# Performance work log

Hardware: AMD Instinct MI355X
Metric: run time of the kernel (lower is better)

The kernel has to match this reference:

```python
import jax, jax.numpy as jnp
import numpy as np
import math

H = 16
D_MODEL = 1024
D_K = D_MODEL // H


def setup_inputs() -> dict:
    key = jax.random.key(0)
    ks = jax.random.split(key, 11)
    B, S, D = 4, 2048, D_MODEL
    scale = 1.0 / math.sqrt(D)
    inp = {
        "query": jax.random.normal(ks[0], (B, S, D), jnp.float32),
        "key": jax.random.normal(ks[1], (B, S, D), jnp.float32),
        "value": jax.random.normal(ks[2], (B, S, D), jnp.float32),
        # four Linear(d_model, d_model) layers: Wq, Wk, Wv, Wo (weights stored [in, out])
        "Wq": jax.random.normal(ks[3], (D, D), jnp.float32) * scale,
        "bq": jnp.zeros((D,), jnp.float32),
        "Wk": jax.random.normal(ks[4], (D, D), jnp.float32) * scale,
        "bk": jnp.zeros((D,), jnp.float32),
        "Wv": jax.random.normal(ks[5], (D, D), jnp.float32) * scale,
        "bv": jnp.zeros((D,), jnp.float32),
        "Wo": jax.random.normal(ks[6], (D, D), jnp.float32) * scale,
        "bo": jnp.zeros((D,), jnp.float32),
    }
    return inp


def reference(query, key, value, Wq, bq, Wk, bk, Wv, bv, Wo, bo):
    B, S, D = query.shape
    # QKV projections, split into heads: [B, H, S, d_k]
    def proj(x, W, b):
        return (x @ W + b).reshape(B, -1, H, D_K).transpose(0, 2, 1, 3)

    q = proj(query, Wq, bq)
    k = proj(key, Wk, bk)
    v = proj(value, Wv, bv)

    # scaled dot-product attention (mask=None, dropout p=0 -> identity)
    scores = jnp.einsum("bhqd,bhkd->bhqk", q, k) / math.sqrt(D_K)
    p_attn = jax.nn.softmax(scores, axis=-1)
    x = jnp.einsum("bhqk,bhkd->bhqd", p_attn, v)

    # merge heads and output projection
    x = x.transpose(0, 2, 1, 3).reshape(B, -1, H * D_K)
    return x @ Wo + bo
```

## Files before the change

kernel.cpp:

```cpp
#include <hip/hip_runtime.h>


typedef unsigned short u16;
typedef unsigned int u32;
typedef __attribute__((ext_vector_type(8))) short bfx8;
typedef __attribute__((ext_vector_type(4))) float f32x4;
typedef __attribute__((ext_vector_type(16))) float f32x16;
typedef __attribute__((ext_vector_type(4))) float fx4;
typedef __attribute__((ext_vector_type(8))) u16 u16x8;
typedef __attribute__((ext_vector_type(4))) u16 u16x4;
typedef __attribute__((ext_vector_type(4))) u32 u32x4;

__device__ __forceinline__ u16 f2bf(float f) {
  union { float f; u32 u; } v; v.f = f;
  u32 u = v.u;
  u += 0x7fffu + ((u >> 16) & 1u);
  return (u16)(u >> 16);
}

__device__ __forceinline__ u32 cvtpk(float a, float b) {
  u32 r;
  asm("v_cvt_pk_bf16_f32 %0, %1, %2" : "=v"(r) : "v"(a), "v"(b));
  return r;
}

__device__ __forceinline__ void gl_lds16(const void* g, void* l) {
  __builtin_amdgcn_global_load_lds((const __attribute__((address_space(1))) void*)g,
                                   (__attribute__((address_space(3))) void*)l, 16, 0, 0);
}

__global__ void prep(const float* __restrict__ q, const float* __restrict__ k,
                     const float* __restrict__ v, u16* __restrict__ inBase,
                     const float* __restrict__ W0, const float* __restrict__ W1,
                     const float* __restrict__ W2, const float* __restrict__ W3,
                     u16* __restrict__ WtBase) {
  __shared__ float tile[64][65];
  const int bid = blockIdx.x;
  const int t = threadIdx.x;
  if (bid < 12288) {
    const int z = bid >> 12, xb = bid & 4095;
    const float* in = z == 0 ? q : (z == 1 ? k : v);
    u16* out = inBase + (size_t)z * (8192ull * 1024);
    const int i = (xb * 256 + t) * 8;
    fx4 a = *(const fx4*)(in + i);
    fx4 b = *(const fx4*)(in + i + 4);
    u16x8 o;
    o[0] = f2bf(a[0]); o[1] = f2bf(a[1]); o[2] = f2bf(a[2]); o[3] = f2bf(a[3]);
    o[4] = f2bf(b[0]); o[5] = f2bf(b[1]); o[6] = f2bf(b[2]); o[7] = f2bf(b[3]);
    *(u16x8*)(out + i) = o;
  } else {
    const int wb = bid - 12288;
    const int z = wb >> 8, rem = wb & 255;
    const float* W = z == 0 ? W0 : (z == 1 ? W1 : (z == 2 ? W2 : W3));
    u16* Wt = WtBase + (size_t)z * (1024ull * 1024);
    const int n0 = (rem & 15) << 6, k0 = (rem >> 4) << 6;
    {
      int r = t >> 2, c = (t & 3) << 4;
      const float* src = W + (size_t)(k0 + r) * 1024 + n0 + c;
#pragma unroll
      for (int u = 0; u < 4; ++u) {
        fx4 vv = *(const fx4*)(src + u * 4);
        tile[r][c + u * 4 + 0] = vv[0];
        tile[r][c + u * 4 + 1] = vv[1];
        tile[r][c + u * 4 + 2] = vv[2];
        tile[r][c + u * 4 + 3] = vv[3];
      }
    }
    __syncthreads();
    {
      int nn = t >> 2, j = t & 3;
      u16x8 o0, o1;
#pragma unroll
      for (int e = 0; e < 8; ++e) o0[e] = f2bf(tile[(j << 4) + e][nn]);
#pragma unroll
      for (int e = 0; e < 8; ++e) o1[e] = f2bf(tile[(j << 4) + 8 + e][nn]);
      u16* dst = Wt + (size_t)(n0 + nn) * 1024 + k0 + (j << 4);
      *(u16x8*)dst = o0;
      *(u16x8*)(dst + 8) = o1;
    }
  }
}

template <int EPI>
__device__ __forceinline__ void gemm_body(const u16* __restrict__ A, const u16* __restrict__ Bt,
                                          const float* __restrict__ bias, void* __restrict__ out,
                                          float scale, char* smem, int m0, int n0) {
  const int t = threadIdx.x;
  const int w = t >> 6, l = t & 63;
  const int lg = l >> 4, lr = l & 15;
  const int wr = w >> 1, wc = w & 1;

  f32x4 acc[4][4] = {};

  const int trow = t >> 3;
  const int scb = ((t & 7) << 4) ^ ((trow & 7) << 4);
  const char* gA = (const char*)A + (size_t)(m0 + trow) * 2048;
  const char* gB = (const char*)Bt + (size_t)(n0 + trow) * 2048;

#define GSTAGE(kt, buf)                                                        \
  do {                                                                         \
    _Pragma("unroll")                                                          \
    for (int i = 0; i < 4; ++i) {                                              \
      gl_lds16(gA + (size_t)i * 32 * 2048 + ((kt) << 7) + scb,                 \
               (buf) + (((i << 8) + (w << 6)) << 4));                          \
      gl_lds16(gB + (size_t)i * 32 * 2048 + ((kt) << 7) + scb,                 \
               (buf) + 16384 + (((i << 8) + (w << 6)) << 4));                  \
    }                                                                          \
  } while (0)

  GSTAGE(0, smem);
  __syncthreads();

  for (int kt = 0; kt < 16; ++kt) {
    char* sA = smem + ((kt & 1) << 15);
    char* sB = sA + 16384;
    if (kt < 15) GSTAGE(kt + 1, smem + (((kt + 1) & 1) << 15));

#pragma unroll
    for (int kk = 0; kk < 2; ++kk) {
      const int off = ((kk << 6) + (lg << 4)) ^ ((lr & 7) << 4);
      bfx8 av[4], bv[4];
#pragma unroll
      for (int fi = 0; fi < 4; ++fi)
        av[fi] = *(const bfx8*)(sA + ((wr << 6) + (fi << 4) + lr) * 128 + off);
#pragma unroll
      for (int fj = 0; fj < 4; ++fj)
        bv[fj] = *(const bfx8*)(sB + ((wc << 6) + (fj << 4) + lr) * 128 + off);
#pragma unroll
      for (int fi = 0; fi < 4; ++fi)
#pragma unroll
        for (int fj = 0; fj < 4; ++fj)
          acc[fi][fj] = __builtin_amdgcn_mfma_f32_16x16x32_bf16(av[fi], bv[fj], acc[fi][fj], 0, 0, 0);
    }
    __syncthreads();
  }
#undef GSTAGE

#pragma unroll
  for (int fj = 0; fj < 4; ++fj) {
    const int n = n0 + (wc << 6) + (fj << 4) + lr;
    const float bvl = bias[n];
#pragma unroll
    for (int fi = 0; fi < 4; ++fi) {
      if constexpr (EPI == 2) {
        const int h = n >> 6, d = n & 63;
        const int mm = m0 + (wr << 6) + (fi << 4) + (lg << 2);
        const int b = mm >> 11, s = mm & 2047;
        u16x4 pk4;
#pragma unroll
        for (int r = 0; r < 4; ++r) pk4[r] = f2bf(acc[fi][fj][r] + bvl);
        *(u16x4*)((u16*)out + (size_t)(b * 16 + h) * 131072 + (size_t)d * 2048 + s) = pk4;
      } else {
#pragma unroll
        for (int r = 0; r < 4; ++r) {
          const int m = m0 + (wr << 6) + (fi << 4) + (lg << 2) + r;
          const float val = (acc[fi][fj][r] + bvl) * scale;
          if constexpr (EPI == 0) {
            const int b = m >> 11, s = m & 2047, h = n >> 6, d = n & 63;
            ((u16*)out)[(((size_t)(b * 16 + h) * 2048 + s) << 6) + d] = f2bf(val);
          } else {
            ((float*)out)[((size_t)m << 10) + n] = val;
          }
        }
      }
    }
  }
}

__device__ __forceinline__ void xcd_remap(int& m0, int& n0) {
  const int lin = blockIdx.x + (blockIdx.y << 3);
  const int c = lin & 7, j = lin >> 3;
  m0 = (((j & 7) << 3) + c) << 7;
  n0 = (j >> 3) << 7;
}

__global__ void __launch_bounds__(256, 2)
gemm_qkv(const u16* __restrict__ A0, const u16* __restrict__ Wt0,
         const float* __restrict__ bq, const float* __restrict__ bk,
         const float* __restrict__ bv, u16* __restrict__ out0, u16* __restrict__ vt) {
  __shared__ __align__(16) char smem[65536];
  const int z = blockIdx.z;
  int m0, n0;
  xcd_remap(m0, n0);
  const u16* A = A0 + (size_t)z * (8192ull * 1024);
  const u16* Bt = Wt0 + (size_t)z * (1024ull * 1024);
  if (z == 2) {
    gemm_body<2>(A, Bt, bv, vt, 1.0f, smem, m0, n0);
  } else {
    const float* bias = z == 0 ? bq : bk;
    const float scale = z == 0 ? 0.18033688011112042f : 1.0f;
    gemm_body<0>(A, Bt, bias, out0 + (size_t)z * (8192ull * 1024), scale, smem, m0, n0);
  }
}

__global__ void __launch_bounds__(256, 2)
gemm_o(const u16* __restrict__ A, const u16* __restrict__ Bt,
       const float* __restrict__ bias, float* __restrict__ out) {
  __shared__ __align__(16) char smem[65536];
  int m0, n0;
  xcd_remap(m0, n0);
  gemm_body<1>(A, Bt, bias, out, 1.0f, smem, m0, n0);
}

__global__ void __launch_bounds__(512, 4)
attn_fwd(const u16* __restrict__ Qg, const u16* __restrict__ Kg,
         const u16* __restrict__ Vtg, u16* __restrict__ Og) {
  __shared__ __align__(16) char smem[65536];
  const int t = threadIdx.x;
  const int w = t >> 6, l = t & 63;
  const int l31 = l & 31, hi = l >> 5;

  const int id = blockIdx.x;
  const int xcd = id & 7, slot = id >> 3;
  const int pair = ((slot >> 3) << 3) + xcd;
  const int q0 = (slot & 7) << 8;

  const char* Qb = (const char*)Qg + ((size_t)pair << 18);
  const char* Kb = (const char*)Kg + ((size_t)pair << 18);
  const char* Vb = (const char*)Vtg + ((size_t)pair << 18);

  const int trow = t >> 3;
  const int scb = (((t & 7) ^ (trow & 7) ^ (((trow >> 3) & 3) << 1)) << 4);
  const int ldst = (w << 10);
  const int swz = (((l & 7) ^ ((l31 >> 3) << 1)) << 4);

  bfx8 qf[4];
#pragma unroll
  for (int ks = 0; ks < 4; ++ks)
    qf[ks] = *(const bfx8*)(Qb + (size_t)(q0 + (w << 5) + l31) * 128 + (ks << 5) + (hi << 4));

  f32x16 accO[2] = {};
  float Lp = 0.f;

#define ASTAGE(kt, buf)                                                         \
  do {                                                                          \
    gl_lds16(Kb + (size_t)(kt) * 8192 + (size_t)trow * 128 + scb, (buf) + ldst);\
    gl_lds16(Vb + (size_t)trow * 4096 + (size_t)(kt) * 128 + scb,               \
             (buf) + 8192 + ldst);                                              \
  } while (0)

  ASTAGE(0, smem);
  ASTAGE(1, smem + 16384);
  __syncthreads();

  for (int it2 = 0; it2 < 16; ++it2) {
    const int tt = it2 << 1;
    if (tt + 2 < 32) ASTAGE(tt + 2, smem + (((tt + 2) & 3) << 14));
    if (tt + 3 < 32) ASTAGE(tt + 3, smem + (((tt + 3) & 3) << 14));

#pragma unroll
    for (int u = 0; u < 2; ++u) {
      char* bK = smem + (((tt + u) & 3) << 14);
      char* bV = bK + 8192;

      f32x16 accS[2] = {{}, {}};
      __builtin_amdgcn_s_setprio(1);
#pragma unroll
      for (int mb = 0; mb < 2; ++mb) {
        bfx8 kf[4];
#pragma unroll
        for (int ks = 0; ks < 4; ++ks)
          kf[ks] = *(const bfx8*)(bK + (((mb << 5) + l31) << 7) + (((ks << 5) + (hi << 4)) ^ swz));
#pragma unroll
        for (int ks = 0; ks < 4; ++ks)
          accS[mb] = __builtin_amdgcn_mfma_f32_32x32x16_bf16(kf[ks], qf[ks], accS[mb], 0, 0, 0);
      }
      __builtin_amdgcn_s_setprio(0);

      bfx8 pa[4];
#pragma unroll
      for (int mb = 0; mb < 2; ++mb) {
#pragma unroll
        for (int r = 0; r < 16; ++r) {
          accS[mb][r] = __builtin_amdgcn_exp2f(accS[mb][r]);
          Lp += accS[mb][r];
        }
#pragma unroll
        for (int half = 0; half < 2; ++half) {
          u32 a0 = cvtpk(accS[mb][8 * half + 0], accS[mb][8 * half + 1]);
          u32 a1 = cvtpk(accS[mb][8 * half + 2], accS[mb][8 * half + 3]);
          u32 b0 = cvtpk(accS[mb][8 * half + 4], accS[mb][8 * half + 5]);
          u32 b1 = cvtpk(accS[mb][8 * half + 6], accS[mb][8 * half + 7]);
          asm volatile("v_permlane32_swap_b32 %0, %1" : "+v"(a0), "+v"(b0));
          asm volatile("v_permlane32_swap_b32 %0, %1" : "+v"(a1), "+v"(b1));
          u32x4 pk; pk[0] = a0; pk[1] = a1; pk[2] = b0; pk[3] = b1;
          pa[(mb << 1) + half] = *(bfx8*)&pk;
        }
      }

      __builtin_amdgcn_s_setprio(1);
#pragma unroll
      for (int ks = 0; ks < 4; ++ks) {
        bfx8 vf0 = *(const bfx8*)(bV + ((0 + l31) << 7) + (((ks << 5) + (hi << 4)) ^ swz));
        bfx8 vf1 = *(const bfx8*)(bV + ((32 + l31) << 7) + (((ks << 5) + (hi << 4)) ^ swz));
        accO[0] = __builtin_amdgcn_mfma_f32_32x32x16_bf16(pa[ks], vf0, accO[0], 0, 0, 0);
        accO[1] = __builtin_amdgcn_mfma_f32_32x32x16_bf16(pa[ks], vf1, accO[1], 0, 0, 0);
      }
      __builtin_amdgcn_s_setprio(0);
    }

    __syncthreads();
  }
#undef ASTAGE

  const float Ltot = Lp + __shfl_xor(Lp, 32);
  const int b = pair >> 4, h = pair & 15;
  u16* dstBase = Og + (((size_t)(b * 2048 + q0 + (w << 5))) << 10) + (h << 6) + l31;
#pragma unroll
  for (int r = 0; r < 16; ++r) {
    const int ql = (r & 3) + ((r >> 2) << 3) + (hi << 2);
    const float Lr = __shfl(Ltot, ql);
    const float rinv = __builtin_amdgcn_rcpf(Lr);
    u16* dst = dstBase + ((size_t)ql << 10);
    dst[0]  = f2bf(accO[0][r] * rinv);
    dst[32] = f2bf(accO[1][r] * rinv);
  }
}

extern "C" void kernel_launch(void* const* d_in, const int* in_sizes, int n_in,
                              void* d_out, int out_size, void* d_ws, size_t ws_size,
                              hipStream_t stream) {
  const float* q  = (const float*)d_in[0];
  const float* k  = (const float*)d_in[1];
  const float* v  = (const float*)d_in[2];
  const float* Wq = (const float*)d_in[3];
  const float* bq = (const float*)d_in[4];
  const float* Wk = (const float*)d_in[5];
  const float* bk = (const float*)d_in[6];
  const float* Wv = (const float*)d_in[7];
  const float* bv = (const float*)d_in[8];
  const float* Wo = (const float*)d_in[9];
  const float* bo = (const float*)d_in[10];
  float* out = (float*)d_out;
  char* ws = (char*)d_ws;

  const size_t MB = 1024 * 1024;
  if (ws_size < 104 * MB) return;

  u16* inq = (u16*)(ws + 0 * MB);
  u16* wqt = (u16*)(ws + 48 * MB);
  u16* wot = (u16*)(ws + 54 * MB);
  u16* Qh  = (u16*)(ws + 56 * MB);
  u16* Kh  = (u16*)(ws + 72 * MB);
  u16* Vth = (u16*)(ws + 88 * MB);
  u16* Ob  = inq;

  prep<<<13312, 256, 0, stream>>>(q, k, v, inq, Wq, Wk, Wv, Wo, wqt);
  gemm_qkv<<<dim3(8, 64, 3), 256, 0, stream>>>(inq, wqt, bq, bk, bv, Qh, Vth);
  attn_fwd<<<512, 512, 0, stream>>>(Qh, Kh, Vth, Ob);
  gemm_o<<<dim3(8, 64), 256, 0, stream>>>(Ob, wot, bo, out);
}
```

Measured before the change: 182.4 us.

## Software-pipeline attention loop to overlap QK^T of next tile with PV of previous

Restructures the attention main loop so each iteration issues the QK^T MFMAs for the current K tile back to back with the PV MFMAs for the previous tile's softmax output, then computes exp and packing afterwards. This gives the matrix cores independent work while the exp/convert/permlane sequence runs, and removes the strict QK->softmax->PV dependency within one tile. The prefetch schedule changes from two tiles every two iterations to one tile per iteration, with a prologue and epilogue and a barrier on every tile, which doubles the number of __syncthreads and may add register pressure since pa stays live across iterations.

After: 205.5 us. 12.7% more time.

```diff
diff --git a/kernel.cpp b/kernel.cpp
--- a/kernel.cpp
+++ b/kernel.cpp
@@ -231,6 +231,7 @@
 
   f32x16 accO[2] = {};
   float Lp = 0.f;
+  bfx8 pa[4];
 
 #define ASTAGE(kt, buf)                                                         \
   do {                                                                          \
@@ -239,69 +240,93 @@
              (buf) + 8192 + ldst);                                              \
   } while (0)
 
+#define QKT(accS, bufK)                                                         \
+  do {                                                                          \
+    _Pragma("unroll")                                                           \
+    for (int mb = 0; mb < 2; ++mb) {                                            \
+      bfx8 kf[4];                                                               \
+      _Pragma("unroll")                                                         \
+      for (int ks = 0; ks < 4; ++ks)                                            \
+        kf[ks] = *(const bfx8*)((bufK) + (((mb << 5) + l31) << 7) +             \
+                                (((ks << 5) + (hi << 4)) ^ swz));               \
+      _Pragma("unroll")                                                         \
+      for (int ks = 0; ks < 4; ++ks)                                            \
+        accS[mb] = __builtin_amdgcn_mfma_f32_32x32x16_bf16(kf[ks], qf[ks],      \
+                                                           accS[mb], 0, 0, 0);  \
+    }                                                                           \
+  } while (0)
+
+#define SOFTMAX(accS)                                                           \
+  do {                                                                          \
+    _Pragma("unroll")                                                           \
+    for (int mb = 0; mb < 2; ++mb) {                                            \
+      _Pragma("unroll")                                                         \
+      for (int r = 0; r < 16; ++r) {                                            \
+        accS[mb][r] = __builtin_amdgcn_exp2f(accS[mb][r]);                      \
+        Lp += accS[mb][r];                                                      \
+      }                                                                         \
+      _Pragma("unroll")                                                         \
+      for (int half = 0; half < 2; ++half) {                                    \
+        u32 a0 = cvtpk(accS[mb][8 * half + 0], accS[mb][8 * half + 1]);         \
+        u32 a1 = cvtpk(accS[mb][8 * half + 2], accS[mb][8 * half + 3]);         \
+        u32 b0 = cvtpk(accS[mb][8 * half + 4], accS[mb][8 * half + 5]);         \
+        u32 b1 = cvtpk(accS[mb][8 * half + 6], accS[mb][8 * half + 7]);         \
+        asm volatile("v_permlane32_swap_b32 %0, %1" : "+v"(a0), "+v"(b0));      \
+        asm volatile("v_permlane32_swap_b32 %0, %1" : "+v"(a1), "+v"(b1));      \
+        u32x4 pk; pk[0] = a0; pk[1] = a1; pk[2] = b0; pk[3] = b1;               \
+        pa[(mb << 1) + half] = *(bfx8*)&pk;                                     \
+      }                                                                         \
+    }                                                                           \
+  } while (0)
+
+#define PV(bufV)                                                                \
+  do {                                                                          \
+    _Pragma("unroll")                                                           \
+    for (int ks = 0; ks < 4; ++ks) {                                            \
+      bfx8 vf0 = *(const bfx8*)((bufV) + ((0 + l31) << 7) +                     \
+                                (((ks << 5) + (hi << 4)) ^ swz));               \
+      bfx8 vf1 = *(const bfx8*)((bufV) + ((32 + l31) << 7) +                    \
+                                (((ks << 5) + (hi << 4)) ^ swz));               \
+      accO[0] = __builtin_amdgcn_mfma_f32_32x32x16_bf16(pa[ks], vf0, accO[0], 0, 0, 0); \
+      accO[1] = __builtin_amdgcn_mfma_f32_32x32x16_bf16(pa[ks], vf1, accO[1], 0, 0, 0); \
+    }                                                                           \
+  } while (0)
+
   ASTAGE(0, smem);
   ASTAGE(1, smem + 16384);
   __syncthreads();
 
-  for (int it2 = 0; it2 < 16; ++it2) {
-    const int tt = it2 << 1;
-    if (tt + 2 < 32) ASTAGE(tt + 2, smem + (((tt + 2) & 3) << 14));
-    if (tt + 3 < 32) ASTAGE(tt + 3, smem + (((tt + 3) & 3) << 14));
-
-#pragma unroll
-    for (int u = 0; u < 2; ++u) {
-      char* bK = smem + (((tt + u) & 3) << 14);
-      char* bV = bK + 8192;
-
-      f32x16 accS[2] = {{}, {}};
-      __builtin_amdgcn_s_setprio(1);
-#pragma unroll
-      for (int mb = 0; mb < 2; ++mb) {
-        bfx8 kf[4];
-#pragma unroll
-        for (int ks = 0; ks < 4; ++ks)
-          kf[ks] = *(const bfx8*)(bK + (((mb << 5) + l31) << 7) + (((ks << 5) + (hi << 4)) ^ swz));
-#pragma unroll
-        for (int ks = 0; ks < 4; ++ks)
-          accS[mb] = __builtin_amdgcn_mfma_f32_32x32x16_bf16(kf[ks], qf[ks], accS[mb], 0, 0, 0);
-      }
-      __builtin_amdgcn_s_setprio(0);
-
-      bfx8 pa[4];
-#pragma unroll
-      for (int mb = 0; mb < 2; ++mb) {
-#pragma unroll
-        for (int r = 0; r < 16; ++r) {
-          accS[mb][r] = __builtin_amdgcn_exp2f(accS[mb][r]);
-          Lp += accS[mb][r];
-        }
-#pragma unroll
-        for (int half = 0; half < 2; ++half) {
-          u32 a0 = cvtpk(accS[mb][8 * half + 0], accS[mb][8 * half + 1]);
-          u32 a1 = cvtpk(accS[mb][8 * half + 2], accS[mb][8 * half + 3]);
-          u32 b0 = cvtpk(accS[mb][8 * half + 4], accS[mb][8 * half + 5]);
-          u32 b1 = cvtpk(accS[mb][8 * half + 6], accS[mb][8 * half + 7]);
-          asm volatile("v_permlane32_swap_b32 %0, %1" : "+v"(a0), "+v"(b0));
-          asm volatile("v_permlane32_swap_b32 %0, %1" : "+v"(a1), "+v"(b1));
-          u32x4 pk; pk[0] = a0; pk[1] = a1; pk[2] = b0; pk[3] = b1;
-          pa[(mb << 1) + half] = *(bfx8*)&pk;
-        }
-      }
-
-      __builtin_amdgcn_s_setprio(1);
-#pragma unroll
-      for (int ks = 0; ks < 4; ++ks) {
-        bfx8 vf0 = *(const bfx8*)(bV + ((0 + l31) << 7) + (((ks << 5) + (hi << 4)) ^ swz));
-        bfx8 vf1 = *(const bfx8*)(bV + ((32 + l31) << 7) + (((ks << 5) + (hi << 4)) ^ swz));
-        accO[0] = __builtin_amdgcn_mfma_f32_32x32x16_bf16(pa[ks], vf0, accO[0], 0, 0, 0);
-        accO[1] = __builtin_amdgcn_mfma_f32_32x32x16_bf16(pa[ks], vf1, accO[1], 0, 0, 0);
-      }
-      __builtin_amdgcn_s_setprio(0);
-    }
+  {
+    f32x16 accS[2] = {{}, {}};
+    __builtin_amdgcn_s_setprio(1);
+    QKT(accS, smem);
+    __builtin_amdgcn_s_setprio(0);
+    SOFTMAX(accS);
+  }
+  __syncthreads();
+
+  for (int it = 1; it < 32; ++it) {
+    char* bK = smem + ((it & 3) << 14);
+    char* bVprev = smem + (((it - 1) & 3) << 14) + 8192;
+    if (it < 31) ASTAGE(it + 1, smem + (((it + 1) & 3) << 14));
+
+    f32x16 accS[2] = {{}, {}};
+    __builtin_amdgcn_s_setprio(1);
+    QKT(accS, bK);
+    PV(bVprev);
+    __builtin_amdgcn_s_setprio(0);
+    SOFTMAX(accS);
 
     __syncthreads();
   }
+
+  __builtin_amdgcn_s_setprio(1);
+  PV(smem + ((31 & 3) << 14) + 8192);
+  __builtin_amdgcn_s_setprio(0);
 #undef ASTAGE
+#undef QKT
+#undef SOFTMAX
+#undef PV
 
   const float Ltot = Lp + __shfl_xor(Lp, 32);
   const int b = pair >> 4, h = pair & 15;
```

## Fuse fp32-to-bf16 activation conversion into QKV GEMM A-tile loading

Applied to the files above, without the earlier changes.

The separate prep pass that converted the fp32 query/key/value activations to bf16 is removed. The QKV GEMM now loads fp32 A tiles into registers, converts them with v_cvt_pk_bf16_f32, and writes them into swizzled LDS, prefetching the next tile while the MFMAs run. Only the weight transpose stays as its own kernel. This avoids writing and re-reading a 48MB bf16 intermediate, but the GEMM now reads fp32 A (twice the bytes per tile), uses register staging instead of direct global-to-LDS loads, and needs more VGPRs.

After: 206.1 us. 1.13x slower.

```diff
diff --git a/kernel.cpp b/kernel.cpp
--- a/kernel.cpp
+++ b/kernel.cpp
@@ -9,6 +9,7 @@
 typedef __attribute__((ext_vector_type(4))) float fx4;
 typedef __attribute__((ext_vector_type(8))) u16 u16x8;
 typedef __attribute__((ext_vector_type(4))) u16 u16x4;
+typedef __attribute__((ext_vector_type(2))) u32 u32x2;
 typedef __attribute__((ext_vector_type(4))) u32 u32x4;
 
 __device__ __forceinline__ u16 f2bf(float f) {
@@ -29,62 +30,174 @@
                                    (__attribute__((address_space(3))) void*)l, 16, 0, 0);
 }
 
-__global__ void prep(const float* __restrict__ q, const float* __restrict__ k,
-                     const float* __restrict__ v, u16* __restrict__ inBase,
-                     const float* __restrict__ W0, const float* __restrict__ W1,
-                     const float* __restrict__ W2, const float* __restrict__ W3,
-                     u16* __restrict__ WtBase) {
+__global__ void wtrans4(const float* __restrict__ W0, const float* __restrict__ W1,
+                        const float* __restrict__ W2, const float* __restrict__ W3,
+                        u16* __restrict__ WtBase) {
   __shared__ float tile[64][65];
-  const int bid = blockIdx.x;
+  const int z = blockIdx.z;
+  const float* W = z == 0 ? W0 : (z == 1 ? W1 : (z == 2 ? W2 : W3));
+  u16* Wt = WtBase + (size_t)z * (1024ull * 1024);
   const int t = threadIdx.x;
-  if (bid < 12288) {
-    const int z = bid >> 12, xb = bid & 4095;
-    const float* in = z == 0 ? q : (z == 1 ? k : v);
-    u16* out = inBase + (size_t)z * (8192ull * 1024);
-    const int i = (xb * 256 + t) * 8;
-    fx4 a = *(const fx4*)(in + i);
-    fx4 b = *(const fx4*)(in + i + 4);
-    u16x8 o;
-    o[0] = f2bf(a[0]); o[1] = f2bf(a[1]); o[2] = f2bf(a[2]); o[3] = f2bf(a[3]);
-    o[4] = f2bf(b[0]); o[5] = f2bf(b[1]); o[6] = f2bf(b[2]); o[7] = f2bf(b[3]);
-    *(u16x8*)(out + i) = o;
-  } else {
-    const int wb = bid - 12288;
-    const int z = wb >> 8, rem = wb & 255;
-    const float* W = z == 0 ? W0 : (z == 1 ? W1 : (z == 2 ? W2 : W3));
-    u16* Wt = WtBase + (size_t)z * (1024ull * 1024);
-    const int n0 = (rem & 15) << 6, k0 = (rem >> 4) << 6;
-    {
-      int r = t >> 2, c = (t & 3) << 4;
-      const float* src = W + (size_t)(k0 + r) * 1024 + n0 + c;
-#pragma unroll
-      for (int u = 0; u < 4; ++u) {
-        fx4 vv = *(const fx4*)(src + u * 4);
-        tile[r][c + u * 4 + 0] = vv[0];
-        tile[r][c + u * 4 + 1] = vv[1];
-        tile[r][c + u * 4 + 2] = vv[2];
-        tile[r][c + u * 4 + 3] = vv[3];
+  const int n0 = blockIdx.x << 6, k0 = blockIdx.y << 6;
+  {
+    int r = t >> 2, c = (t & 3) << 4;
+    const float* src = W + (size_t)(k0 + r) * 1024 + n0 + c;
+#pragma unroll
+    for (int u = 0; u < 4; ++u) {
+      fx4 vv = *(const fx4*)(src + u * 4);
+      tile[r][c + u * 4 + 0] = vv[0];
+      tile[r][c + u * 4 + 1] = vv[1];
+      tile[r][c + u * 4 + 2] = vv[2];
+      tile[r][c + u * 4 + 3] = vv[3];
+    }
+  }
+  __syncthreads();
+  {
+    int nn = t >> 2, j = t & 3;
+    u16x8 o0, o1;
+#pragma unroll
+    for (int e = 0; e < 8; ++e) o0[e] = f2bf(tile[(j << 4) + e][nn]);
+#pragma unroll
+    for (int e = 0; e < 8; ++e) o1[e] = f2bf(tile[(j << 4) + 8 + e][nn]);
+    u16* dst = Wt + (size_t)(n0 + nn) * 1024 + k0 + (j << 4);
+    *(u16x8*)dst = o0;
+    *(u16x8*)(dst + 8) = o1;
+  }
+}
+
+__device__ __forceinline__ void xcd_remap(int& m0, int& n0) {
+  const int lin = blockIdx.x + (blockIdx.y << 3);
+  const int c = lin & 7, j = lin >> 3;
+  m0 = (((j & 7) << 3) + c) << 7;
+  n0 = (j >> 3) << 7;
+}
+
+__global__ void __launch_bounds__(256, 2)
+gemm_qkvf(const float* __restrict__ qf32, const float* __restrict__ kf32,
+          const float* __restrict__ vf32, const u16* __restrict__ Wt0,
+          const float* __restrict__ bq, const float* __restrict__ bk,
+          const float* __restrict__ bv, u16* __restrict__ out0, u16* __restrict__ vt) {
+  __shared__ __align__(16) char smem[65536];
+  const int z = blockIdx.z;
+  int m0, n0;
+  xcd_remap(m0, n0);
+  const float* A = z == 0 ? qf32 : (z == 1 ? kf32 : vf32);
+  const u16* Bt = Wt0 + (size_t)z * (1024ull * 1024);
+  const float* bias = z == 0 ? bq : (z == 1 ? bk : bv);
+  const float scale = z == 0 ? 0.18033688011112042f : 1.0f;
+
+  const int t = threadIdx.x;
+  const int w = t >> 6, l = t & 63;
+  const int lg = l >> 4, lr = l & 15;
+  const int wr = w >> 1, wc = w & 1;
+
+  f32x4 acc[4][4] = {};
+
+  const int arow = t >> 4;
+  const int acol = t & 15;
+  const float* gAf = A + (size_t)(m0 + arow) * 1024 + (acol << 2);
+  const int woff = ((((acol >> 1) ^ (arow & 7)) << 4) + ((acol & 1) << 3));
+
+  const int trow = t >> 3;
+  const int scb = ((t & 7) << 4) ^ ((trow & 7) << 4);
+  const char* gB = (const char*)Bt + (size_t)(n0 + trow) * 2048;
+
+  fx4 areg[8];
+
+#define ALOAD(kt)                                                              \
+  do {                                                                         \
+    _Pragma("unroll")                                                          \
+    for (int p = 0; p < 8; ++p)                                                \
+      areg[p] = *(const fx4*)(gAf + (size_t)p * 16 * 1024 + ((kt) << 6));      \
+  } while (0)
+
+#define AWRITE(buf)                                                            \
+  do {                                                                         \
+    _Pragma("unroll")                                                          \
+    for (int p = 0; p < 8; ++p) {                                              \
+      u32x2 pk2;                                                               \
+      pk2[0] = cvtpk(areg[p][0], areg[p][1]);                                  \
+      pk2[1] = cvtpk(areg[p][2], areg[p][3]);                                  \
+      *(u32x2*)((buf) + (((p << 4) + arow) << 7) + woff) = pk2;                \
+    }                                                                          \
+  } while (0)
+
+#define BSTAGE(kt, buf)                                                        \
+  do {                                                                         \
+    _Pragma("unroll")                                                          \
+    for (int i = 0; i < 4; ++i)                                                \
+      gl_lds16(gB + (size_t)i * 32 * 2048 + ((kt) << 7) + scb,                 \
+               (buf) + 16384 + (((i << 8) + (w << 6)) << 4));                  \
+  } while (0)
+
+  ALOAD(0);
+  BSTAGE(0, smem);
+  AWRITE(smem);
+  __syncthreads();
+
+  for (int kt = 0; kt < 16; ++kt) {
+    char* sA = smem + ((kt & 1) << 15);
+    char* sB = sA + 16384;
+    char* nb = smem + (((kt + 1) & 1) << 15);
+    if (kt < 15) { ALOAD(kt + 1); BSTAGE(kt + 1, nb); }
+
+#pragma unroll
+    for (int kk = 0; kk < 2; ++kk) {
+      const int off = ((kk << 6) + (lg << 4)) ^ ((lr & 7) << 4);
+      bfx8 av[4], bv4[4];
+#pragma unroll
+      for (int fi = 0; fi < 4; ++fi)
+        av[fi] = *(const bfx8*)(sA + ((wr << 6) + (fi << 4) + lr) * 128 + off);
+#pragma unroll
+      for (int fj = 0; fj < 4; ++fj)
+        bv4[fj] = *(const bfx8*)(sB + ((wc << 6) + (fj << 4) + lr) * 128 + off);
+#pragma unroll
+      for (int fi = 0; fi < 4; ++fi)
+#pragma unroll
+        for (int fj = 0; fj < 4; ++fj)
+          acc[fi][fj] = __builtin_amdgcn_mfma_f32_16x16x32_bf16(av[fi], bv4[fj], acc[fi][fj], 0, 0, 0);
+    }
+    if (kt < 15) AWRITE(nb);
+    __syncthreads();
+  }
+#undef ALOAD
+#undef AWRITE
+#undef BSTAGE
+
+#pragma unroll
+  for (int fj = 0; fj < 4; ++fj) {
+    const int n = n0 + (wc << 6) + (fj << 4) + lr;
+    const float bvl = bias[n];
+#pragma unroll
+    for (int fi = 0; fi < 4; ++fi) {
+      if (z == 2) {
+        const int h = n >> 6, d = n & 63;
+        const int mm = m0 + (wr << 6) + (fi << 4) + (lg << 2);
+        const int b = mm >> 11, s = mm & 2047;
+        u16x4 pk4;
+#pragma unroll
+        for (int r = 0; r < 4; ++r) pk4[r] = f2bf(acc[fi][fj][r] + bvl);
+        *(u16x4*)(vt + (size_t)(b * 16 + h) * 131072 + (size_t)d * 2048 + s) = pk4;
+      } else {
+#pragma unroll
+        for (int r = 0; r < 4; ++r) {
+          const int m = m0 + (wr << 6) + (fi << 4) + (lg << 2) + r;
+          const float val = (acc[fi][fj][r] + bvl) * scale;
+          const int b = m >> 11, s = m & 2047, h = n >> 6, d = n & 63;
+          out0[(size_t)z * (8192ull * 1024) +
+               (((size_t)(b * 16 + h) * 2048 + s) << 6) + d] = f2bf(val);
+        }
       }
     }
-    __syncthreads();
-    {
-      int nn = t >> 2, j = t & 3;
-      u16x8 o0, o1;
-#pragma unroll
-      for (int e = 0; e < 8; ++e) o0[e] = f2bf(tile[(j << 4) + e][nn]);
-#pragma unroll
-      for (int e = 0; e < 8; ++e) o1[e] = f2bf(tile[(j << 4) + 8 + e][nn]);
-      u16* dst = Wt + (size_t)(n0 + nn) * 1024 + k0 + (j << 4);
-      *(u16x8*)dst = o0;
-      *(u16x8*)(dst + 8) = o1;
-    }
-  }
-}
-
-template <int EPI>
-__device__ __forceinline__ void gemm_body(const u16* __restrict__ A, const u16* __restrict__ Bt,
-                                          const float* __restrict__ bias, void* __restrict__ out,
-                                          float scale, char* smem, int m0, int n0) {
+  }
+}
+
+__global__ void __launch_bounds__(256, 2)
+gemm_o(const u16* __restrict__ A, const u16* __restrict__ Bt,
+       const float* __restrict__ bias, float* __restrict__ out) {
+  __shared__ __align__(16) char smem[65536];
+  int m0, n0;
+  xcd_remap(m0, n0);
   const int t = threadIdx.x;
   const int w = t >> 6, l = t & 63;
   const int lg = l >> 4, lr = l & 15;
@@ -119,18 +232,18 @@
 #pragma unroll
     for (int kk = 0; kk < 2; ++kk) {
       const int off = ((kk << 6) + (lg << 4)) ^ ((lr & 7) << 4);
-      bfx8 av[4], bv[4];
+      bfx8 av[4], bv4[4];
 #pragma unroll
       for (int fi = 0; fi < 4; ++fi)
         av[fi] = *(const bfx8*)(sA + ((wr << 6) + (fi << 4) + lr) * 128 + off);
 #pragma unroll
       for (int fj = 0; fj < 4; ++fj)
-        bv[fj] = *(const bfx8*)(sB + ((wc << 6) + (fj << 4) + lr) * 128 + off);
+        bv4[fj] = *(const bfx8*)(sB + ((wc << 6) + (fj << 4) + lr) * 128 + off);
 #pragma unroll
       for (int fi = 0; fi < 4; ++fi)
 #pragma unroll
         for (int fj = 0; fj < 4; ++fj)
-          acc[fi][fj] = __builtin_amdgcn_mfma_f32_16x16x32_bf16(av[fi], bv[fj], acc[fi][fj], 0, 0, 0);
+          acc[fi][fj] = __builtin_amdgcn_mfma_f32_16x16x32_bf16(av[fi], bv4[fj], acc[fi][fj], 0, 0, 0);
     }
     __syncthreads();
   }
@@ -142,64 +255,13 @@
     const float bvl = bias[n];
 #pragma unroll
     for (int fi = 0; fi < 4; ++fi) {
-      if constexpr (EPI == 2) {
-        const int h = n >> 6, d = n & 63;
-        const int mm = m0 + (wr << 6) + (fi << 4) + (lg << 2);
-        const int b = mm >> 11, s = mm & 2047;
-        u16x4 pk4;
-#pragma unroll
-        for (int r = 0; r < 4; ++r) pk4[r] = f2bf(acc[fi][fj][r] + bvl);
-        *(u16x4*)((u16*)out + (size_t)(b * 16 + h) * 131072 + (size_t)d * 2048 + s) = pk4;
-      } else {
-#pragma unroll
-        for (int r = 0; r < 4; ++r) {
-          const int m = m0 + (wr << 6) + (fi << 4) + (lg << 2) + r;
-          const float val = (acc[fi][fj][r] + bvl) * scale;
-          if constexpr (EPI == 0) {
-            const int b = m >> 11, s = m & 2047, h = n >> 6, d = n & 63;
-            ((u16*)out)[(((size_t)(b * 16 + h) * 2048 + s) << 6) + d] = f2bf(val);
-          } else {
-            ((float*)out)[((size_t)m << 10) + n] = val;
-          }
-        }
+#pragma unroll
+      for (int r = 0; r < 4; ++r) {
+        const int m = m0 + (wr << 6) + (fi << 4) + (lg << 2) + r;
+        out[((size_t)m << 10) + n] = acc[fi][fj][r] + bvl;
       }
     }
   }
-}
-
-__device__ __forceinline__ void xcd_remap(int& m0, int& n0) {
-  const int lin = blockIdx.x + (blockIdx.y << 3);
-  const int c = lin & 7, j = lin >> 3;
-  m0 = (((j & 7) << 3) + c) << 7;
-  n0 = (j >> 3) << 7;
-}
-
-__global__ void __launch_bounds__(256, 2)
-gemm_qkv(const u16* __restrict__ A0, const u16* __restrict__ Wt0,
-         const float* __restrict__ bq, const float* __restrict__ bk,
-         const float* __restrict__ bv, u16* __restrict__ out0, u16* __restrict__ vt) {
-  __shared__ __align__(16) char smem[65536];
-  const int z = blockIdx.z;
-  int m0, n0;
-  xcd_remap(m0, n0);
-  const u16* A = A0 + (size_t)z * (8192ull * 1024);
-  const u16* Bt = Wt0 + (size_t)z * (1024ull * 1024);
-  if (z == 2) {
-    gemm_body<2>(A, Bt, bv, vt, 1.0f, smem, m0, n0);
-  } else {
-    const float* bias = z == 0 ? bq : bk;
-    const float scale = z == 0 ? 0.18033688011112042f : 1.0f;
-    gemm_body<0>(A, Bt, bias, out0 + (size_t)z * (8192ull * 1024), scale, smem, m0, n0);
-  }
-}
-
-__global__ void __launch_bounds__(256, 2)
-gemm_o(const u16* __restrict__ A, const u16* __restrict__ Bt,
-       const float* __restrict__ bias, float* __restrict__ out) {
-  __shared__ __align__(16) char smem[65536];
-  int m0, n0;
-  xcd_remap(m0, n0);
-  gemm_body<1>(A, Bt, bias, out, 1.0f, smem, m0, n0);
 }
 
 __global__ void __launch_bounds__(512, 4)
@@ -337,16 +399,15 @@
   const size_t MB = 1024 * 1024;
   if (ws_size < 104 * MB) return;
 
-  u16* inq = (u16*)(ws + 0 * MB);
+  u16* Ob  = (u16*)(ws + 0 * MB);
   u16* wqt = (u16*)(ws + 48 * MB);
   u16* wot = (u16*)(ws + 54 * MB);
   u16* Qh  = (u16*)(ws + 56 * MB);
   u16* Kh  = (u16*)(ws + 72 * MB);
   u16* Vth = (u16*)(ws + 88 * MB);
-  u16* Ob  = inq;
-
-  prep<<<13312, 256, 0, stream>>>(q, k, v, inq, Wq, Wk, Wv, Wo, wqt);
-  gemm_qkv<<<dim3(8, 64, 3), 256, 0, stream>>>(inq, wqt, bq, bk, bv, Qh, Vth);
+
+  wtrans4<<<dim3(16, 16, 4), 256, 0, stream>>>(Wq, Wk, Wv, Wo, wqt);
+  gemm_qkvf<<<dim3(8, 64, 3), 256, 0, stream>>>(q, k, v, wqt, bq, bk, bv, Qh, Vth);
   attn_fwd<<<512, 512, 0, stream>>>(Qh, Kh, Vth, Ob);
   gemm_o<<<dim3(8, 64), 256, 0, stream>>>(Ob, wot, bo, out);
 }
```

## Halve GEMM K-tile to 32 and double occupancy to four blocks per CU

Applied to the files above, without the earlier changes.

The projection GEMMs now stage 32-wide K tiles (64 bytes per row) instead of 64, using a new XOR swizzle for the 64-byte rows and 32 K iterations. Shared memory per block drops from 64KB to 32KB, and launch bounds rise to 4 blocks per CU. The aim is more concurrent blocks to hide global-to-LDS latency, at the cost of twice as many barriers per K and a tighter register budget of 128 VGPRs.

After: 199.9 us. 1.1x slower.

```diff
diff --git a/kernel.cpp b/kernel.cpp
--- a/kernel.cpp
+++ b/kernel.cpp
@@ -92,46 +92,43 @@
 
   f32x4 acc[4][4] = {};
 
-  const int trow = t >> 3;
-  const int scb = ((t & 7) << 4) ^ ((trow & 7) << 4);
-  const char* gA = (const char*)A + (size_t)(m0 + trow) * 2048;
-  const char* gB = (const char*)Bt + (size_t)(n0 + trow) * 2048;
+  const int srow = t >> 2;
+  const int sc = (((t & 3) ^ ((t >> 2) & 3) ^ ((t >> 4) & 3)) << 4);
+  const char* gA = (const char*)A + (size_t)(m0 + srow) * 2048 + sc;
+  const char* gB = (const char*)Bt + (size_t)(n0 + srow) * 2048 + sc;
+  const int ldsb = (w << 10);
 
 #define GSTAGE(kt, buf)                                                        \
   do {                                                                         \
-    _Pragma("unroll")                                                          \
-    for (int i = 0; i < 4; ++i) {                                              \
-      gl_lds16(gA + (size_t)i * 32 * 2048 + ((kt) << 7) + scb,                 \
-               (buf) + (((i << 8) + (w << 6)) << 4));                          \
-      gl_lds16(gB + (size_t)i * 32 * 2048 + ((kt) << 7) + scb,                 \
-               (buf) + 16384 + (((i << 8) + (w << 6)) << 4));                  \
-    }                                                                          \
+    gl_lds16(gA + ((kt) << 6), (buf) + ldsb);                                  \
+    gl_lds16(gA + (size_t)64 * 2048 + ((kt) << 6), (buf) + 4096 + ldsb);       \
+    gl_lds16(gB + ((kt) << 6), (buf) + 8192 + ldsb);                           \
+    gl_lds16(gB + (size_t)64 * 2048 + ((kt) << 6), (buf) + 12288 + ldsb);      \
   } while (0)
+
+  const int off = ((lg ^ (lr & 3) ^ ((lr >> 2) & 3)) << 4);
 
   GSTAGE(0, smem);
   __syncthreads();
 
-  for (int kt = 0; kt < 16; ++kt) {
-    char* sA = smem + ((kt & 1) << 15);
-    char* sB = sA + 16384;
-    if (kt < 15) GSTAGE(kt + 1, smem + (((kt + 1) & 1) << 15));
-
-#pragma unroll
-    for (int kk = 0; kk < 2; ++kk) {
-      const int off = ((kk << 6) + (lg << 4)) ^ ((lr & 7) << 4);
-      bfx8 av[4], bv[4];
-#pragma unroll
-      for (int fi = 0; fi < 4; ++fi)
-        av[fi] = *(const bfx8*)(sA + ((wr << 6) + (fi << 4) + lr) * 128 + off);
+  for (int kt = 0; kt < 32; ++kt) {
+    char* sA = smem + ((kt & 1) << 14);
+    char* sB = sA + 8192;
+    if (kt < 31) GSTAGE(kt + 1, smem + (((kt + 1) & 1) << 14));
+
+    bfx8 av[4], bv4[4];
+#pragma unroll
+    for (int fi = 0; fi < 4; ++fi)
+      av[fi] = *(const bfx8*)(sA + (((wr << 6) + (fi << 4) + lr) << 6) + off);
+#pragma unroll
+    for (int fj = 0; fj < 4; ++fj)
+      bv4[fj] = *(const bfx8*)(sB + (((wc << 6) + (fj << 4) + lr) << 6) + off);
+#pragma unroll
+    for (int fi = 0; fi < 4; ++fi)
 #pragma unroll
       for (int fj = 0; fj < 4; ++fj)
-        bv[fj] = *(const bfx8*)(sB + ((wc << 6) + (fj << 4) + lr) * 128 + off);
-#pragma unroll
-      for (int fi = 0; fi < 4; ++fi)
-#pragma unroll
-        for (int fj = 0; fj < 4; ++fj)
-          acc[fi][fj] = __builtin_amdgcn_mfma_f32_16x16x32_bf16(av[fi], bv[fj], acc[fi][fj], 0, 0, 0);
-    }
+        acc[fi][fj] = __builtin_amdgcn_mfma_f32_16x16x32_bf16(av[fi], bv4[fj], acc[fi][fj], 0, 0, 0);
+
     __syncthreads();
   }
 #undef GSTAGE
@@ -174,11 +171,11 @@
   n0 = (j >> 3) << 7;
 }
 
-__global__ void __launch_bounds__(256, 2)
+__global__ void __launch_bounds__(256, 4)
 gemm_qkv(const u16* __restrict__ A0, const u16* __restrict__ Wt0,
          const float* __restrict__ bq, const float* __restrict__ bk,
          const float* __restrict__ bv, u16* __restrict__ out0, u16* __restrict__ vt) {
-  __shared__ __align__(16) char smem[65536];
+  __shared__ __align__(16) char smem[32768];
   const int z = blockIdx.z;
   int m0, n0;
   xcd_remap(m0, n0);
@@ -193,10 +190,10 @@
   }
 }
 
-__global__ void __launch_bounds__(256, 2)
+__global__ void __launch_bounds__(256, 4)
 gemm_o(const u16* __restrict__ A, const u16* __restrict__ Bt,
        const float* __restrict__ bias, float* __restrict__ out) {
-  __shared__ __align__(16) char smem[65536];
+  __shared__ __align__(16) char smem[32768];
   int m0, n0;
   xcd_remap(m0, n0);
   gemm_body<1>(A, Bt, bias, out, 1.0f, smem, m0, n0);
```
